# Optimization experiments

Hardware: AMD Instinct MI355X
Metric: run time of the kernel (lower is better)

Reference implementation:

```python
import jax, jax.numpy as jnp
import numpy as np

N, E = 20000, 320000
IN_DIM, EDGE_DIM, HID = 64, 16, 64
# (in_c, heads, channels, out_c) per layer; last layer heads=1, concat=False
DIMS = [(64, 4, 64, 256), (256, 4, 64, 256), (256, 1, 64, 64)]


def _ln(x, g, b):
    m = x.mean(-1, keepdims=True)
    v = x.var(-1, keepdims=True)
    return (x - m) / jnp.sqrt(v + 1e-5) * g + b


def _gatv2(x, ei, ea, Wl, bl, Wr, br, We, att, bc, concat):
    # PyG GATv2Conv, eval mode (no dropout), add_self_loops=True, fill_value='mean'
    n = x.shape[0]
    H, C = att.shape
    ar = jnp.arange(n, dtype=ei.dtype)
    src = jnp.concatenate([ei[0], ar])
    dst = jnp.concatenate([ei[1], ar])
    ea_f = jnp.concatenate([ea, jnp.broadcast_to(ea.mean(0), (n, ea.shape[1]))], 0)
    xl = (x @ Wl + bl).reshape(n, H, C)   # source transform
    xr = (x @ Wr + br).reshape(n, H, C)   # target transform
    ee = (ea_f @ We).reshape(-1, H, C)    # edge transform (no bias in PyG)
    e = jax.nn.leaky_relu(xl[src] + xr[dst] + ee, 0.2)       # [E+N, H, C]
    score = jnp.einsum('ehc,hc->eh', e, att)                 # [E+N, H]
    mx = jax.ops.segment_max(score, dst, num_segments=n)
    a = jnp.exp(score - mx[dst])
    a = a / (jax.ops.segment_sum(a, dst, num_segments=n)[dst] + 1e-16)
    out = jax.ops.segment_sum(a[:, :, None] * xl[src], dst, num_segments=n)  # [N,H,C]
    out = out.reshape(n, H * C) if concat else out.mean(1)
    return out + bc


def _forward(x, eis, eas, Wp, bp, gp, bep, layers):
    h = jax.nn.gelu(_ln(x @ Wp + bp, gp, bep), approximate=False)
    for i in range(3):
        Wl, bl, Wr, br, We, att, bc, g, be, Wsk, bsk = layers[i]
        res = h @ Wsk + bsk
        h = _gatv2(h, eis[i], eas[i], Wl, bl, Wr, br, We, att, bc, i < 2)
        h = jax.nn.gelu(_ln(h, g, be), approximate=False) + res
    return h


def setup_inputs() -> dict:
    key = jax.random.key(0)
    ks = iter(jax.random.split(key, 64))
    rn = lambda shape, s=0.05: jax.random.normal(next(ks), shape, jnp.float32) * s
    d = {'x': jax.random.normal(next(ks), (N, IN_DIM), jnp.float32)}
    for i in range(3):
        d['ei%d' % i] = jax.random.randint(next(ks), (2, E), 0, N, jnp.int32)
        d['ea%d' % i] = jax.random.normal(next(ks), (E, EDGE_DIM), jnp.float32)
    d['Wp'] = rn((IN_DIM, HID)); d['bp'] = jnp.zeros(HID)
    d['gp'] = jnp.ones(HID); d['bep'] = jnp.zeros(HID)
    for i, (ic, H, C, oc) in enumerate(DIMS):
        hc = H * C
        d['Wl%d' % i] = rn((ic, hc)); d['bl%d' % i] = jnp.zeros(hc)
        d['Wr%d' % i] = rn((ic, hc)); d['br%d' % i] = jnp.zeros(hc)
        d['We%d' % i] = rn((EDGE_DIM, hc))
        d['att%d' % i] = rn((H, C), 0.1)
        d['bc%d' % i] = jnp.zeros(hc if i < 2 else C)
        d['g%d' % i] = jnp.ones(oc); d['be%d' % i] = jnp.zeros(oc)
        d['Wsk%d' % i] = rn((ic, oc)); d['bsk%d' % i] = jnp.zeros(oc)
    return d


def reference(x, ei0, ea0, ei1, ea1, ei2, ea2, Wp, bp, gp, bep,
              Wl0, bl0, Wr0, br0, We0, att0, bc0, g0, be0, Wsk0, bsk0,
              Wl1, bl1, Wr1, br1, We1, att1, bc1, g1, be1, Wsk1, bsk1,
              Wl2, bl2, Wr2, br2, We2, att2, bc2, g2, be2, Wsk2, bsk2):
    layers = [
        (Wl0, bl0, Wr0, br0, We0, att0, bc0, g0, be0, Wsk0, bsk0),
        (Wl1, bl1, Wr1, br1, We1, att1, bc1, g1, be1, Wsk1, bsk1),
        (Wl2, bl2, Wr2, br2, We2, att2, bc2, g2, be2, Wsk2, bsk2),
    ]
    return _forward(x, (ei0, ei1, ei2), (ea0, ea1, ea2), Wp, bp, gp, bep, layers)
```

## Files before the change

kernel.cpp:

```cpp
#include <hip/hip_runtime.h>
#include <hip/hip_bf16.h>
#include <math.h>

#define NV 20000
#define NE 320000
#define CSR_PAD 8

typedef __attribute__((ext_vector_type(8))) short bf16x8;
typedef __attribute__((ext_vector_type(4))) float f32x4;
typedef __attribute__((ext_vector_type(2))) _Float16 h2;

static __device__ __forceinline__ ushort f2b(float f) {
  __hip_bfloat16 h = __float2bfloat16(f);
  return *reinterpret_cast<ushort*>(&h);
}
static __device__ __forceinline__ float b2f(ushort u) {
  union { ushort s[2]; float f; } c;
  c.s[0] = 0; c.s[1] = u;
  return c.f;
}
static __device__ __forceinline__ ushort f2h(float f) {
  _Float16 h = (_Float16)f;
  return *reinterpret_cast<ushort*>(&h);
}
static __device__ __forceinline__ float blo(unsigned u) { return __uint_as_float(u << 16); }
static __device__ __forceinline__ float bhi(unsigned u) { return __uint_as_float(u & 0xffff0000u); }

static __device__ __forceinline__ float wave_sum64(float x) {
  x += __int_as_float(__builtin_amdgcn_update_dpp(0, __float_as_int(x), 0x111, 0xF, 0xF, true));
  x += __int_as_float(__builtin_amdgcn_update_dpp(0, __float_as_int(x), 0x112, 0xF, 0xF, true));
  x += __int_as_float(__builtin_amdgcn_update_dpp(0, __float_as_int(x), 0x114, 0xF, 0xF, true));
  x += __int_as_float(__builtin_amdgcn_update_dpp(0, __float_as_int(x), 0x118, 0xF, 0xF, true));
  x += __int_as_float(__builtin_amdgcn_update_dpp(0, __float_as_int(x), 0x142, 0xA, 0xF, true));
  x += __int_as_float(__builtin_amdgcn_update_dpp(0, __float_as_int(x), 0x143, 0xC, 0xF, true));
  return __int_as_float(__builtin_amdgcn_readlane(__float_as_int(x), 63));
}

static __device__ __forceinline__ float sum16(float x) {
  x += __int_as_float(__builtin_amdgcn_update_dpp(0, __float_as_int(x), 0x121, 0xF, 0xF, true));
  x += __int_as_float(__builtin_amdgcn_update_dpp(0, __float_as_int(x), 0x122, 0xF, 0xF, true));
  x += __int_as_float(__builtin_amdgcn_update_dpp(0, __float_as_int(x), 0x124, 0xF, 0xF, true));
  x += __int_as_float(__builtin_amdgcn_update_dpp(0, __float_as_int(x), 0x128, 0xF, 0xF, true));
  return x;
}

static __device__ __forceinline__ float dot16h(const uint4* __restrict__ E,
                                               const h2* __restrict__ Wch) {
#if __has_builtin(__builtin_amdgcn_fdot2)
  const h2* e = (const h2*)E;
  float s = 0.f;
#pragma unroll
  for (int j = 0; j < 8; ++j) s = __builtin_amdgcn_fdot2(e[j], Wch[j], s, false);
  return s;
#else
  const unsigned* u = (const unsigned*)E;
  float s = 0.f;
#pragma unroll
  for (int j = 0; j < 8; ++j) {
    union { unsigned v; h2 h; } cv; cv.v = u[j];
    s = fmaf((float)cv.h[0], (float)Wch[j][0], s);
    s = fmaf((float)cv.h[1], (float)Wch[j][1], s);
  }
  return s;
#endif
}

struct CJob { const float* src; ushort* dst; int K, M; };
struct PrepArgs {
  const int* ei[3];
  const float* ea[3];
  int* counts[3];
  float* easum[3];
  CJob jobs[9];
  const float *x, *Wp, *bp, *gp, *bep;
  ushort* h0;
};

__global__ __launch_bounds__(256) void prep_kernel(PrepArgs a) {
  const int y = blockIdx.y, t = threadIdx.x;
  if (y < 3) {
    if (blockIdx.x < 256) {
      const float4* ea4 = (const float4*)a.ea[y];
      const int cg = t & 3;
      int r = blockIdx.x * 64 + (t >> 2);
      const int rstride = 256 * 64;
      float4 s = make_float4(0.f, 0.f, 0.f, 0.f);
      for (; r < NE; r += rstride) {
        float4 v = ea4[(size_t)r * 4 + cg];
        s.x += v.x; s.y += v.y; s.z += v.z; s.w += v.w;
      }
      __shared__ float4 red4[256];
      red4[t] = s;
      __syncthreads();
      if (t < 4) {
        float4 tot = make_float4(0.f, 0.f, 0.f, 0.f);
        for (int j = t; j < 256; j += 4) {
          float4 v = red4[j];
          tot.x += v.x; tot.y += v.y; tot.z += v.z; tot.w += v.w;
        }
        atomicAdd(&a.easum[y][t * 4 + 0], tot.x);
        atomicAdd(&a.easum[y][t * 4 + 1], tot.y);
        atomicAdd(&a.easum[y][t * 4 + 2], tot.z);
        atomicAdd(&a.easum[y][t * 4 + 3], tot.w);
      }
    }
    int i = blockIdx.x * 256 + t;
    if (i < NE) atomicAdd(&a.counts[y][a.ei[y][NE + i]], 1);
  } else if (y == 3) {
#pragma unroll
    for (int j = 0; j < 9; ++j) {
      CJob jb = a.jobs[j];
      const int total = jb.M * jb.K;
      for (int i = blockIdx.x * 256 + t; i < total; i += gridDim.x * 256) {
        int m = i / jb.K, k = i - m * jb.K;
        jb.dst[i] = f2b(jb.src[(size_t)k * jb.M + m]);
      }
    }
  } else {
    int wid = t >> 6, lane = t & 63;
    for (int row = blockIdx.x * 4 + wid; row < NV; row += gridDim.x * 4) {
      float xv = a.x[(size_t)row * 64 + lane];
      float acc = a.bp[lane];
#pragma unroll
      for (int k = 0; k < 64; ++k) {
        float v = __shfl(xv, k, 64);
        acc = fmaf(v, a.Wp[k * 64 + lane], acc);
      }
      float s1 = wave_sum64(acc), s2 = wave_sum64(acc * acc);
      float mean = s1 * (1.0f / 64.0f);
      float var  = s2 * (1.0f / 64.0f) - mean * mean;
      float yv = (acc - mean) * rsqrtf(var + 1e-5f) * a.gp[lane] + a.bep[lane];
      float gel = 0.5f * yv * (1.0f + erff(yv * 0.70710678118654752f));
      a.h0[(size_t)row * 64 + lane] = f2b(gel);
    }
  }
}

__global__ __launch_bounds__(1024) void scan_kernel(
    int* __restrict__ countsA, int* __restrict__ cursorA)
{
  int* counts = countsA + blockIdx.x * (NV + 1);
  int* cursor = cursorA + blockIdx.x * NV;
  __shared__ int ws[16];
  __shared__ int wexcl[17];
  const int t = threadIdx.x, lane = t & 63, wid = t >> 6;
  const int base = t * 20;
  int v[20];
  int tot = 0;
#pragma unroll
  for (int j = 0; j < 20; ++j) {
    int i = base + j;
    v[j] = (i < NV) ? counts[i] : 0;
    tot += v[j];
  }
  int x = tot;
#pragma unroll
  for (int o = 1; o < 64; o <<= 1) {
    int yy = __shfl_up(x, o, 64);
    if (lane >= o) x += yy;
  }
  if (lane == 63) ws[wid] = x;
  __syncthreads();
  if (t == 0) {
    int r = 0;
#pragma unroll
    for (int j = 0; j < 16; ++j) { wexcl[j] = r; r += ws[j]; }
    wexcl[16] = r;
  }
  __syncthreads();
  int run = wexcl[wid] + (x - tot);
#pragma unroll
  for (int j = 0; j < 20; ++j) {
    int i = base + j;
    if (i < NV) { counts[i] = run; cursor[i] = run; }
    run += v[j];
  }
  if (t == 0) counts[NV] = wexcl[16];
}

struct G0SArgs {
  const ushort *A, *WT;
  const float *b0, *b1, *b2;
  ushort *O0, *O1; float* O2;
  int K, M1, M2, Mtot, NT;
  const int* ei[3]; const float* ea[3];
  int* cursor;
  unsigned* csr[3]; ushort* eab[3]; int HC[3];
};

__global__ __launch_bounds__(256) void gemm0_scatter_kernel(G0SArgs a) {
  __shared__ ushort As[128][40];
  __shared__ ushort Bs[64][40];
  const int t = threadIdx.x;
  if ((int)blockIdx.x < a.NT) {
    const int wave = t >> 6, lane = t & 63;
    const int mcols = a.Mtot >> 6;
    const int col0 = ((int)blockIdx.x % mcols) * 64, row0 = ((int)blockIdx.x / mcols) * 128;
    const int m_ = lane & 15, q = lane >> 4;
    f32x4 acc[2][4];
#pragma unroll
    for (int i = 0; i < 2; ++i)
#pragma unroll
      for (int j = 0; j < 4; ++j) acc[i][j] = (f32x4){0.f, 0.f, 0.f, 0.f};
    const int ar = t >> 1, ac = (t & 1) * 16;
    const int br = t >> 2, bcol = (t & 3) * 8;
    const ushort* Ap = a.A + (size_t)(row0 + ar) * a.K + ac;
    const ushort* Bp = a.WT + (size_t)(col0 + br) * a.K + bcol;
    const bool a_ok = (row0 + ar) < NV;
    for (int k0 = 0; k0 < a.K; k0 += 32) {
      uint4 av0 = make_uint4(0, 0, 0, 0), av1 = make_uint4(0, 0, 0, 0);
      if (a_ok) { av0 = *(const uint4*)(Ap + k0); av1 = *(const uint4*)(Ap + k0 + 8); }
      uint4 bv = *(const uint4*)(Bp + k0);
      *(uint4*)&As[ar][ac] = av0;
      *(uint4*)&As[ar][ac + 8] = av1;
      *(uint4*)&Bs[br][bcol] = bv;
      __syncthreads();
      bf16x8 a0 = *(const bf16x8*)&As[wave * 32 + m_][q * 8];
      bf16x8 a1 = *(const bf16x8*)&As[wave * 32 + 16 + m_][q * 8];
#pragma unroll
      for (int cf = 0; cf < 4; ++cf) {
        bf16x8 b = *(const bf16x8*)&Bs[cf * 16 + m_][q * 8];
        acc[0][cf] = __builtin_amdgcn_mfma_f32_16x16x32_bf16(a0, b, acc[0][cf], 0, 0, 0);
        acc[1][cf] = __builtin_amdgcn_mfma_f32_16x16x32_bf16(a1, b, acc[1][cf], 0, 0, 0);
      }
      __syncthreads();
    }
    const float* bias; int base, mode, Wd;
    if (col0 < a.M1)      { bias = a.b0; base = 0;    mode = 0; Wd = a.M1; }
    else if (col0 < a.M2) { bias = a.b1; base = a.M1; mode = 1; Wd = a.M2 - a.M1; }
    else                  { bias = a.b2; base = a.M2; mode = 2; Wd = a.Mtot - a.M2; }
#pragma unroll
    for (int rf = 0; rf < 2; ++rf) {
#pragma unroll
      for (int cf = 0; cf < 4; ++cf) {
        int col = col0 + cf * 16 + m_ - base;
        float bb = bias[col];
#pragma unroll
        for (int r = 0; r < 4; ++r) {
          int row = row0 + wave * 32 + rf * 16 + q * 4 + r;
          if (row < NV) {
            float v = acc[rf][cf][r] + bb;
            if (mode == 0)      a.O0[(size_t)row * Wd + col] = f2b(v);
            else if (mode == 1) a.O1[(size_t)row * Wd + col] = f2b(v);
            else                a.O2[(size_t)row * Wd + col] = v;
          }
        }
      }
    }
  } else {
    const int per = NE + CSR_PAD;
    int gi = ((int)blockIdx.x - a.NT) * 256 + t;
    if (gi >= 3 * per) return;
    int l = gi / per, i = gi - l * per;
    if (i >= NE) {
      a.csr[l][i] = 0u;
      uint4 z = make_uint4(0, 0, 0, 0);
      *(uint4*)(a.eab[l] + (size_t)i * 16) = z;
      *(uint4*)(a.eab[l] + (size_t)i * 16 + 8) = z;
      return;
    }
    int dst = a.ei[l][NE + i], src = a.ei[l][i];
    int pos = atomicAdd(&a.cursor[(size_t)l * NV + dst], 1);
    a.csr[l][pos] = (unsigned)(src * a.HC[l]);
    const float4* er = (const float4*)(a.ea[l] + (size_t)i * 16);
    float4 q0 = er[0], q1 = er[1], q2 = er[2], q3 = er[3];
    uint4 w0, w1;
    w0.x = (unsigned)f2h(q0.x) | ((unsigned)f2h(q0.y) << 16);
    w0.y = (unsigned)f2h(q0.z) | ((unsigned)f2h(q0.w) << 16);
    w0.z = (unsigned)f2h(q1.x) | ((unsigned)f2h(q1.y) << 16);
    w0.w = (unsigned)f2h(q1.z) | ((unsigned)f2h(q1.w) << 16);
    w1.x = (unsigned)f2h(q2.x) | ((unsigned)f2h(q2.y) << 16);
    w1.y = (unsigned)f2h(q2.z) | ((unsigned)f2h(q2.w) << 16);
    w1.z = (unsigned)f2h(q3.x) | ((unsigned)f2h(q3.y) << 16);
    w1.w = (unsigned)f2h(q3.z) | ((unsigned)f2h(q3.w) << 16);
    *(uint4*)(a.eab[l] + (size_t)pos * 16) = w0;
    *(uint4*)(a.eab[l] + (size_t)pos * 16 + 8) = w1;
  }
}

__global__ __launch_bounds__(256) void gemm_fused(
    const ushort* __restrict__ A, const ushort* __restrict__ WT,
    const float* __restrict__ b0, const float* __restrict__ b1,
    const float* __restrict__ b2,
    ushort* __restrict__ O0, ushort* __restrict__ O1, float* __restrict__ O2,
    int N, int K, int M1, int M2, int Mtot)
{
  __shared__ ushort As[128][40];
  __shared__ ushort Bs[64][40];
  const int t = threadIdx.x, wave = t >> 6, lane = t & 63;
  const int row0 = blockIdx.y * 128, col0 = blockIdx.x * 64;
  const int m_ = lane & 15, q = lane >> 4;
  f32x4 acc[2][4];
#pragma unroll
  for (int i = 0; i < 2; ++i)
#pragma unroll
    for (int j = 0; j < 4; ++j) acc[i][j] = (f32x4){0.f, 0.f, 0.f, 0.f};
  const int ar = t >> 1, ac = (t & 1) * 16;
  const int br = t >> 2, bcol = (t & 3) * 8;
  const ushort* Ap = A + (size_t)(row0 + ar) * K + ac;
  const ushort* Bp = WT + (size_t)(col0 + br) * K + bcol;
  const bool a_ok = (row0 + ar) < N;
  for (int k0 = 0; k0 < K; k0 += 32) {
    uint4 av0 = make_uint4(0, 0, 0, 0), av1 = make_uint4(0, 0, 0, 0);
    if (a_ok) { av0 = *(const uint4*)(Ap + k0); av1 = *(const uint4*)(Ap + k0 + 8); }
    uint4 bv = *(const uint4*)(Bp + k0);
    *(uint4*)&As[ar][ac] = av0;
    *(uint4*)&As[ar][ac + 8] = av1;
    *(uint4*)&Bs[br][bcol] = bv;
    __syncthreads();
    bf16x8 a0 = *(const bf16x8*)&As[wave * 32 + m_][q * 8];
    bf16x8 a1 = *(const bf16x8*)&As[wave * 32 + 16 + m_][q * 8];
#pragma unroll
    for (int cf = 0; cf < 4; ++cf) {
      bf16x8 b = *(const bf16x8*)&Bs[cf * 16 + m_][q * 8];
      acc[0][cf] = __builtin_amdgcn_mfma_f32_16x16x32_bf16(a0, b, acc[0][cf], 0, 0, 0);
      acc[1][cf] = __builtin_amdgcn_mfma_f32_16x16x32_bf16(a1, b, acc[1][cf], 0, 0, 0);
    }
    __syncthreads();
  }
  const float* bias; int base, mode, Wd;
  if (col0 < M1)      { bias = b0; base = 0;  mode = 0; Wd = M1; }
  else if (col0 < M2) { bias = b1; base = M1; mode = 1; Wd = M2 - M1; }
  else                { bias = b2; base = M2; mode = 2; Wd = Mtot - M2; }
#pragma unroll
  for (int rf = 0; rf < 2; ++rf) {
#pragma unroll
    for (int cf = 0; cf < 4; ++cf) {
      int col = col0 + cf * 16 + m_ - base;
      float bb = bias[col];
#pragma unroll
      for (int r = 0; r < 4; ++r) {
        int row = row0 + wave * 32 + rf * 16 + q * 4 + r;
        if (row < N) {
          float v = acc[rf][cf][r] + bb;
          if (mode == 0)      O0[(size_t)row * Wd + col] = f2b(v);
          else if (mode == 1) O1[(size_t)row * Wd + col] = f2b(v);
          else                O2[(size_t)row * Wd + col] = v;
        }
      }
    }
  }
}

__global__ __launch_bounds__(256) void agg4_kernel(
    const ushort* __restrict__ eab, const float* __restrict__ easum,
    const float* __restrict__ We,
    const ushort* __restrict__ xl, const ushort* __restrict__ xr,
    const float* __restrict__ att, const float* __restrict__ bc,
    const float* __restrict__ g, const float* __restrict__ be,
    const float* __restrict__ res,
    const int* __restrict__ offs, const unsigned* __restrict__ csr,
    ushort* __restrict__ houtb, int E)
{
  const int t = threadIdx.x, lane = t & 63, wave = t >> 6;
  const int n = blockIdx.x * 4 + wave;
  const int cb = 4 * lane;
  const size_t rowb = (size_t)n * 256 + cb;
  const float L2E = 1.4426950408889634f;

  float4 atv = *(const float4*)(att + cb);
  float at[4] = {atv.x * L2E, atv.y * L2E, atv.z * L2E, atv.w * L2E};

  h2 Wch[4][8];
  float esf[4] = {0.f, 0.f, 0.f, 0.f};
#pragma unroll
  for (int k = 0; k < 8; ++k) {
    float4 wr0 = *(const float4*)(We + (2 * k) * 256 + cb);
    float4 wr1 = *(const float4*)(We + (2 * k + 1) * 256 + cb);
    const float* w0 = &wr0.x;
    const float* w1 = &wr1.x;
    float e0 = easum[2 * k], e1 = easum[2 * k + 1];
#pragma unroll
    for (int j = 0; j < 4; ++j) {
      esf[j] = fmaf(e0, w0[j], esf[j]);
      esf[j] = fmaf(e1, w1[j], esf[j]);
      Wch[j][k] = (h2){(_Float16)w0[j], (_Float16)w1[j]};
    }
  }
#pragma unroll
  for (int j = 0; j < 4; ++j) esf[j] *= 1.0f / (float)E;

  uint2 qr = *(const uint2*)(xr + rowb);
  float xrv[4] = {blo(qr.x), bhi(qr.x), blo(qr.y), bhi(qr.y)};
  uint2 qn = *(const uint2*)(xl + rowb);
  float xln[4] = {blo(qn.x), bhi(qn.x), blo(qn.y), bhi(qn.y)};

  float p = 0.f;
#pragma unroll
  for (int j = 0; j < 4; ++j) {
    float v = xln[j] + xrv[j] + esf[j];
    v = v > 0.f ? v : 0.2f * v;
    p = fmaf(v, at[j], p);
  }
  float wself = exp2f(sum16(p));
  float acc[4];
#pragma unroll
  for (int j = 0; j < 4; ++j) acc[j] = wself * xln[j];
  float denom = wself;

  const int beg = __builtin_amdgcn_readfirstlane(offs[n]);
  const int end = __builtin_amdgcn_readfirstlane(offs[n + 1]);

  unsigned P[2];
  uint4 EA[2][2];
  uint2 XL[2];
#pragma unroll
  for (int k = 0; k < 2; ++k) {
    P[k] = csr[beg + k];
    const uint4* ep = (const uint4*)(eab + (size_t)(beg + k) * 16);
    EA[k][0] = ep[0]; EA[k][1] = ep[1];
  }
#pragma unroll
  for (int k = 0; k < 2; ++k)
    XL[k] = *(const uint2*)(xl + __builtin_amdgcn_readfirstlane(P[k]) + cb);

  for (int idx = beg; idx < end; idx += 2) {
    unsigned Q[2];
    uint4 EB[2][2];
    uint2 XN[2];
#pragma unroll
    for (int k = 0; k < 2; ++k) Q[k] = csr[idx + 2 + k];
#pragma unroll
    for (int k = 0; k < 2; ++k) {
      const uint4* ep = (const uint4*)(eab + (size_t)(idx + 2 + k) * 16);
      EB[k][0] = ep[0]; EB[k][1] = ep[1];
    }
#pragma unroll
    for (int k = 0; k < 2; ++k)
      XN[k] = *(const uint2*)(xl + __builtin_amdgcn_readfirstlane(Q[k]) + cb);

#pragma unroll
    for (int k = 0; k < 2; ++k) {
      float xf[4] = {blo(XL[k].x), bhi(XL[k].x), blo(XL[k].y), bhi(XL[k].y)};
      float pp = 0.f;
#pragma unroll
      for (int j = 0; j < 4; ++j) {
        float ee = dot16h(EA[k], Wch[j]);
        float v = xf[j] + xrv[j] + ee;
        v = v > 0.f ? v : 0.2f * v;
        pp = fmaf(v, at[j], pp);
      }
      float S = sum16(pp);
      float w = (idx + k < end) ? exp2f(S) : 0.f;
#pragma unroll
      for (int j = 0; j < 4; ++j) acc[j] = fmaf(w, xf[j], acc[j]);
      denom += w;
    }
#pragma unroll
    for (int k = 0; k < 2; ++k) { P[k] = Q[k]; EA[k][0] = EB[k][0]; EA[k][1] = EB[k][1]; XL[k] = XN[k]; }
  }

  const float inv = 1.0f / (denom + 1e-16f);
  float4 bcv = *(const float4*)(bc + cb);
  float out[4];
  out[0] = acc[0] * inv + bcv.x; out[1] = acc[1] * inv + bcv.y;
  out[2] = acc[2] * inv + bcv.z; out[3] = acc[3] * inv + bcv.w;

  float so1 = out[0] + out[1] + out[2] + out[3];
  float so2 = out[0] * out[0] + out[1] * out[1] + out[2] * out[2] + out[3] * out[3];
  float s1 = wave_sum64(so1), s2 = wave_sum64(so2);
  float mean = s1 * (1.0f / 256.0f);
  float var  = s2 * (1.0f / 256.0f) - mean * mean;
  float rstd = rsqrtf(var + 1e-5f);
  float4 gv = *(const float4*)(g + cb);
  float4 bev = *(const float4*)(be + cb);
  float4 rv = *(const float4*)(res + rowb);
  const float* gp = &gv.x; const float* bep = &bev.x; const float* rp = &rv.x;
  ushort ob[4];
#pragma unroll
  for (int j = 0; j < 4; ++j) {
    float y = (out[j] - mean) * rstd * gp[j] + bep[j];
    float gel = 0.5f * y * (1.0f + erff(y * 0.70710678118654752f));
    ob[j] = f2b(gel + rp[j]);
  }
  uint2 ov;
  ov.x = (unsigned)ob[0] | ((unsigned)ob[1] << 16);
  ov.y = (unsigned)ob[2] | ((unsigned)ob[3] << 16);
  *(uint2*)(houtb + rowb) = ov;
}

__global__ __launch_bounds__(256, 4) void agg1_kernel(
    const ushort* __restrict__ eab, const float* __restrict__ easum,
    const float* __restrict__ We,
    const ushort* __restrict__ xl, const ushort* __restrict__ xr,
    const float* __restrict__ att, const float* __restrict__ bc,
    const float* __restrict__ g, const float* __restrict__ be,
    const float* __restrict__ res,
    const int* __restrict__ offs, const unsigned* __restrict__ csr,
    float* __restrict__ houtf, int E)
{
  const int HC = 64;
  const int t = threadIdx.x, lane = t & 63, wave = t >> 6;
  const int n = blockIdx.x * 4 + wave;
  const int c = lane;

  const float xr_t = b2f(xr[(size_t)n * HC + c]);
  const float att_t = att[c] * 1.4426950408889634f;
  float eself = 0.f;
  h2 Wch[8];
#pragma unroll
  for (int j = 0; j < 8; ++j) {
    float w0 = We[(2 * j) * HC + c], w1 = We[(2 * j + 1) * HC + c];
    eself = fmaf(easum[2 * j], w0, eself);
    eself = fmaf(easum[2 * j + 1], w1, eself);
    Wch[j] = (h2){(_Float16)w0, (_Float16)w1};
  }
  eself *= 1.0f / (float)E;

  const float xln = b2f(xl[(size_t)n * HC + c]);
  float vs = xln + xr_t + eself;
  vs = vs > 0.f ? vs : 0.2f * vs;
  const float wself = exp2f(wave_sum64(vs * att_t));
  float acc = wself * xln, denom = wself;

  const int beg = __builtin_amdgcn_readfirstlane(offs[n]);
  const int end = __builtin_amdgcn_readfirstlane(offs[n + 1]);

  unsigned P[4];
  uint4 EA[4][2];
  float XL[4];
#pragma unroll
  for (int k = 0; k < 4; ++k) {
    P[k] = csr[beg + k];
    const uint4* ep = (const uint4*)(eab + (size_t)(beg + k) * 16);
    EA[k][0] = ep[0]; EA[k][1] = ep[1];
  }
#pragma unroll
  for (int k = 0; k < 4; ++k)
    XL[k] = b2f(xl[__builtin_amdgcn_readfirstlane(P[k]) + c]);

  for (int idx = beg; idx < end; idx += 4) {
    unsigned Q[4];
    uint4 EB[4][2];
    float XLN[4];
#pragma unroll
    for (int k = 0; k < 4; ++k) Q[k] = csr[idx + 4 + k];
#pragma unroll
    for (int k = 0; k < 4; ++k) {
      const uint4* ep = (const uint4*)(eab + (size_t)(idx + 4 + k) * 16);
      EB[k][0] = ep[0]; EB[k][1] = ep[1];
    }
#pragma unroll
    for (int k = 0; k < 4; ++k)
      XLN[k] = b2f(xl[__builtin_amdgcn_readfirstlane(Q[k]) + c]);

    float wv[4];
#pragma unroll
    for (int k = 0; k < 4; ++k) {
      float ee = dot16h(EA[k], Wch);
      float v = XL[k] + xr_t + ee;
      v = v > 0.f ? v : 0.2f * v;
      float S = wave_sum64(v * att_t);
      wv[k] = (idx + k < end) ? exp2f(S) : 0.f;
    }
#pragma unroll
    for (int k = 0; k < 4; ++k) { acc = fmaf(wv[k], XL[k], acc); denom += wv[k]; }
#pragma unroll
    for (int k = 0; k < 4; ++k) {
      P[k] = Q[k]; EA[k][0] = EB[k][0]; EA[k][1] = EB[k][1]; XL[k] = XLN[k];
    }
  }

  float out = acc / (denom + 1e-16f) + bc[c];
  float s1 = wave_sum64(out), s2 = wave_sum64(out * out);
  float mean = s1 / (float)HC;
  float var  = s2 / (float)HC - mean * mean;
  float y = (out - mean) * rsqrtf(var + 1e-5f) * g[c] + be[c];
  float gel = 0.5f * y * (1.0f + erff(y * 0.70710678118654752f));
  houtf[(size_t)n * HC + c] = gel + res[(size_t)n * HC + c];
}

extern "C" void kernel_launch(void* const* d_in, const int* in_sizes, int n_in,
                              void* d_out, int out_size, void* d_ws, size_t ws_size,
                              hipStream_t stream)
{
  auto in = [&](int i) { return (const float*)d_in[i]; };

  const int ic[3] = {64, 256, 256}, hc[3] = {256, 256, 64}, oc[3] = {256, 256, 64};
  const int CSRN = NE + CSR_PAD;

  char* w = (char*)d_ws;
  size_t off = 0;
  auto alloc = [&](size_t bytes) { void* p = w + off; off = (off + bytes + 511) & ~(size_t)511; return p; };
  ushort* B1   = (ushort*)alloc((size_t)NV * 256 * 2);
  ushort* B2   = (ushort*)alloc((size_t)NV * 256 * 2);
  float*  B3   = (float*)alloc((size_t)NV * 256 * 4);
  ushort* h0bf = (ushort*)alloc((size_t)NV * 64 * 2);
  ushort* h1bf = (ushort*)alloc((size_t)NV * 256 * 2);
  ushort* h2bf = (ushort*)alloc((size_t)NV * 256 * 2);
  ushort* Wcat[3];
  for (int i = 0; i < 3; ++i)
    Wcat[i] = (ushort*)alloc((size_t)(2 * hc[i] + oc[i]) * ic[i] * 2);
  float*    easumA  = (float*)alloc(3 * 64);
  int*      countsA = (int*)alloc((size_t)3 * (NV + 1) * 4);
  int*      cursorA = (int*)alloc((size_t)3 * NV * 4);
  unsigned* csrA    = (unsigned*)alloc((size_t)3 * CSRN * 4);
  ushort*   eabA    = (ushort*)alloc((size_t)3 * CSRN * 16 * 2);

  hipMemsetAsync(easumA, 0, 512 + (size_t)3 * (NV + 1) * 4, stream);

  PrepArgs pa;
  for (int i = 0; i < 3; ++i) {
    pa.ei[i] = (const int*)d_in[1 + 2 * i];
    pa.ea[i] = in(2 + 2 * i);
    pa.counts[i] = countsA + i * (NV + 1);
    pa.easum[i] = easumA + i * 16;
    pa.jobs[i * 3 + 0] = {in(11 + 11 * i), Wcat[i],                             ic[i], hc[i]};
    pa.jobs[i * 3 + 1] = {in(13 + 11 * i), Wcat[i] + (size_t)hc[i] * ic[i],     ic[i], hc[i]};
    pa.jobs[i * 3 + 2] = {in(20 + 11 * i), Wcat[i] + (size_t)2 * hc[i] * ic[i], ic[i], oc[i]};
  }
  pa.x = in(0); pa.Wp = in(7); pa.bp = in(8); pa.gp = in(9); pa.bep = in(10);
  pa.h0 = h0bf;
  prep_kernel<<<dim3(1344, 5), 256, 0, stream>>>(pa);

  scan_kernel<<<3, 1024, 0, stream>>>(countsA, cursorA);

  G0SArgs ga;
  ga.A = h0bf; ga.WT = Wcat[0];
  ga.b0 = in(12); ga.b1 = in(14); ga.b2 = in(21);
  ga.O0 = B1; ga.O1 = B2; ga.O2 = B3;
  ga.K = 64; ga.M1 = 256; ga.M2 = 512; ga.Mtot = 768;
  ga.NT = (768 / 64) * ((NV + 127) / 128);
  for (int i = 0; i < 3; ++i) {
    ga.ei[i] = (const int*)d_in[1 + 2 * i];
    ga.ea[i] = in(2 + 2 * i);
    ga.csr[i] = csrA + (size_t)i * CSRN;
    ga.eab[i] = eabA + (size_t)i * CSRN * 16;
    ga.HC[i] = hc[i];
  }
  ga.cursor = cursorA;
  const int scat_blocks = (3 * (NE + CSR_PAD) + 255) / 256;
  gemm0_scatter_kernel<<<ga.NT + scat_blocks, 256, 0, stream>>>(ga);

  agg4_kernel<<<NV / 4, 256, 0, stream>>>(
      eabA + 0, easumA + 0, in(15), B1, B2, in(16), in(17), in(18), in(19),
      B3, countsA, csrA, h1bf, NE);

  gemm_fused<<<dim3(768 / 64, (NV + 127) / 128), 256, 0, stream>>>(
      h1bf, Wcat[1], in(23), in(25), in(32), B1, B2, B3, NV, 256, 256, 512, 768);

  agg4_kernel<<<NV / 4, 256, 0, stream>>>(
      eabA + (size_t)CSRN * 16, easumA + 16, in(26), B1, B2, in(27), in(28),
      in(29), in(30), B3, countsA + (NV + 1), csrA + (size_t)CSRN, h2bf, NE);

  gemm_fused<<<dim3(192 / 64, (NV + 127) / 128), 256, 0, stream>>>(
      h2bf, Wcat[2], in(34), in(36), in(43), B1, B2, B3, NV, 256, 64, 128, 192);

  agg1_kernel<<<NV / 4, 256, 0, stream>>>(
      eabA + (size_t)2 * CSRN * 16, easumA + 32, in(37), B1, B2, in(38), in(39),
      in(40), in(41), B3, countsA + 2 * (NV + 1), csrA + (size_t)2 * CSRN,
      (float*)d_out, NE);
}
```

Measured before the change: 539.4 us.

## Keep edge features in original order and gather them via CSR-stored edge ids

```diff
diff --git a/kernel.cpp b/kernel.cpp
--- a/kernel.cpp
+++ b/kernel.cpp
@@ -4,7 +4,7 @@
 
 #define NV 20000
 #define NE 320000
-#define CSR_PAD 8
+#define CSR_PAD 16
 
 typedef __attribute__((ext_vector_type(8))) short bf16x8;
 typedef __attribute__((ext_vector_type(4))) float f32x4;
@@ -71,6 +71,7 @@
   const float* ea[3];
   int* counts[3];
   float* easum[3];
+  ushort* eab[3];
   CJob jobs[9];
   const float *x, *Wp, *bp, *gp, *bep;
   ushort* h0;
@@ -81,6 +82,7 @@
   if (y < 3) {
     if (blockIdx.x < 256) {
       const float4* ea4 = (const float4*)a.ea[y];
+      ushort* eab = a.eab[y];
       const int cg = t & 3;
       int r = blockIdx.x * 64 + (t >> 2);
       const int rstride = 256 * 64;
@@ -88,6 +90,10 @@
       for (; r < NE; r += rstride) {
         float4 v = ea4[(size_t)r * 4 + cg];
         s.x += v.x; s.y += v.y; s.z += v.z; s.w += v.w;
+        uint2 w;
+        w.x = (unsigned)f2h(v.x) | ((unsigned)f2h(v.y) << 16);
+        w.y = (unsigned)f2h(v.z) | ((unsigned)f2h(v.w) << 16);
+        *(uint2*)(eab + (size_t)r * 16 + cg * 4) = w;
       }
       __shared__ float4 red4[256];
       red4[t] = s;
@@ -183,9 +189,9 @@
   const float *b0, *b1, *b2;
   ushort *O0, *O1; float* O2;
   int K, M1, M2, Mtot, NT;
-  const int* ei[3]; const float* ea[3];
+  const int* ei[3];
   int* cursor;
-  unsigned* csr[3]; ushort* eab[3]; int HC[3];
+  uint2* csr[3]; int HC[3];
 };
 
 __global__ __launch_bounds__(256) void gemm0_scatter_kernel(G0SArgs a) {
@@ -253,28 +259,12 @@
     if (gi >= 3 * per) return;
     int l = gi / per, i = gi - l * per;
     if (i >= NE) {
-      a.csr[l][i] = 0u;
-      uint4 z = make_uint4(0, 0, 0, 0);
-      *(uint4*)(a.eab[l] + (size_t)i * 16) = z;
-      *(uint4*)(a.eab[l] + (size_t)i * 16 + 8) = z;
+      a.csr[l][i] = make_uint2(0u, 0u);
       return;
     }
     int dst = a.ei[l][NE + i], src = a.ei[l][i];
     int pos = atomicAdd(&a.cursor[(size_t)l * NV + dst], 1);
-    a.csr[l][pos] = (unsigned)(src * a.HC[l]);
-    const float4* er = (const float4*)(a.ea[l] + (size_t)i * 16);
-    float4 q0 = er[0], q1 = er[1], q2 = er[2], q3 = er[3];
-    uint4 w0, w1;
-    w0.x = (unsigned)f2h(q0.x) | ((unsigned)f2h(q0.y) << 16);
-    w0.y = (unsigned)f2h(q0.z) | ((unsigned)f2h(q0.w) << 16);
-    w0.z = (unsigned)f2h(q1.x) | ((unsigned)f2h(q1.y) << 16);
-    w0.w = (unsigned)f2h(q1.z) | ((unsigned)f2h(q1.w) << 16);
-    w1.x = (unsigned)f2h(q2.x) | ((unsigned)f2h(q2.y) << 16);
-    w1.y = (unsigned)f2h(q2.z) | ((unsigned)f2h(q2.w) << 16);
-    w1.z = (unsigned)f2h(q3.x) | ((unsigned)f2h(q3.y) << 16);
-    w1.w = (unsigned)f2h(q3.z) | ((unsigned)f2h(q3.w) << 16);
-    *(uint4*)(a.eab[l] + (size_t)pos * 16) = w0;
-    *(uint4*)(a.eab[l] + (size_t)pos * 16 + 8) = w1;
+    a.csr[l][pos] = make_uint2((unsigned)(src * a.HC[l]), (unsigned)i);
   }
 }
 
@@ -349,7 +339,7 @@
     const float* __restrict__ att, const float* __restrict__ bc,
     const float* __restrict__ g, const float* __restrict__ be,
     const float* __restrict__ res,
-    const int* __restrict__ offs, const unsigned* __restrict__ csr,
+    const int* __restrict__ offs, const uint2* __restrict__ csr,
     ushort* __restrict__ houtb, int E)
 {
   const int t = threadIdx.x, lane = t & 63, wave = t >> 6;
@@ -401,33 +391,37 @@
   const int beg = __builtin_amdgcn_readfirstlane(offs[n]);
   const int end = __builtin_amdgcn_readfirstlane(offs[n + 1]);
 
-  unsigned P[2];
+  uint2 QS[2];
   uint4 EA[2][2];
   uint2 XL[2];
-#pragma unroll
-  for (int k = 0; k < 2; ++k) {
-    P[k] = csr[beg + k];
-    const uint4* ep = (const uint4*)(eab + (size_t)(beg + k) * 16);
-    EA[k][0] = ep[0]; EA[k][1] = ep[1];
-  }
-#pragma unroll
-  for (int k = 0; k < 2; ++k)
-    XL[k] = *(const uint2*)(xl + __builtin_amdgcn_readfirstlane(P[k]) + cb);
+  {
+    uint2 Q0[2];
+#pragma unroll
+    for (int k = 0; k < 2; ++k) Q0[k] = csr[beg + k];
+#pragma unroll
+    for (int k = 0; k < 2; ++k) QS[k] = csr[beg + 2 + k];
+#pragma unroll
+    for (int k = 0; k < 2; ++k) {
+      const uint4* ep = (const uint4*)(eab +
+          (size_t)__builtin_amdgcn_readfirstlane(Q0[k].y) * 16);
+      EA[k][0] = ep[0]; EA[k][1] = ep[1];
+      XL[k] = *(const uint2*)(xl + __builtin_amdgcn_readfirstlane(Q0[k].x) + cb);
+    }
+  }
 
   for (int idx = beg; idx < end; idx += 2) {
-    unsigned Q[2];
+    uint2 QN[2];
+#pragma unroll
+    for (int k = 0; k < 2; ++k) QN[k] = csr[idx + 4 + k];
     uint4 EB[2][2];
     uint2 XN[2];
 #pragma unroll
-    for (int k = 0; k < 2; ++k) Q[k] = csr[idx + 2 + k];
-#pragma unroll
     for (int k = 0; k < 2; ++k) {
-      const uint4* ep = (const uint4*)(eab + (size_t)(idx + 2 + k) * 16);
+      const uint4* ep = (const uint4*)(eab +
+          (size_t)__builtin_amdgcn_readfirstlane(QS[k].y) * 16);
       EB[k][0] = ep[0]; EB[k][1] = ep[1];
-    }
-#pragma unroll
-    for (int k = 0; k < 2; ++k)
-      XN[k] = *(const uint2*)(xl + __builtin_amdgcn_readfirstlane(Q[k]) + cb);
+      XN[k] = *(const uint2*)(xl + __builtin_amdgcn_readfirstlane(QS[k].x) + cb);
+    }
 
 #pragma unroll
     for (int k = 0; k < 2; ++k) {
@@ -447,7 +441,9 @@
       denom += w;
     }
 #pragma unroll
-    for (int k = 0; k < 2; ++k) { P[k] = Q[k]; EA[k][0] = EB[k][0]; EA[k][1] = EB[k][1]; XL[k] = XN[k]; }
+    for (int k = 0; k < 2; ++k) {
+      EA[k][0] = EB[k][0]; EA[k][1] = EB[k][1]; XL[k] = XN[k]; QS[k] = QN[k];
+    }
   }
 
   const float inv = 1.0f / (denom + 1e-16f);
@@ -486,7 +482,7 @@
     const float* __restrict__ att, const float* __restrict__ bc,
     const float* __restrict__ g, const float* __restrict__ be,
     const float* __restrict__ res,
-    const int* __restrict__ offs, const unsigned* __restrict__ csr,
+    const int* __restrict__ offs, const uint2* __restrict__ csr,
     float* __restrict__ houtf, int E)
 {
   const int HC = 64;
@@ -516,33 +512,41 @@
   const int beg = __builtin_amdgcn_readfirstlane(offs[n]);
   const int end = __builtin_amdgcn_readfirstlane(offs[n + 1]);
 
-  unsigned P[4];
+  uint2 QS[4];
   uint4 EA[4][2];
   float XL[4];
-#pragma unroll
-  for (int k = 0; k < 4; ++k) {
-    P[k] = csr[beg + k];
-    const uint4* ep = (const uint4*)(eab + (size_t)(beg + k) * 16);
-    EA[k][0] = ep[0]; EA[k][1] = ep[1];
-  }
-#pragma unroll
-  for (int k = 0; k < 4; ++k)
-    XL[k] = b2f(xl[__builtin_amdgcn_readfirstlane(P[k]) + c]);
+  {
+    uint2 Q0[4];
+#pragma unroll
+    for (int k = 0; k < 4; ++k) Q0[k] = csr[beg + k];
+#pragma unroll
+    for (int k = 0; k < 4; ++k) QS[k] = csr[beg + 4 + k];
+#pragma unroll
+    for (int k = 0; k < 4; ++k) {
+      const uint4* ep = (const uint4*)(eab +
+          (size_t)__builtin_amdgcn_readfirstlane(Q0[k].y) * 16);
+      EA[k][0] = ep[0]; EA[k][1] = ep[1];
+    }
+#pragma unroll
+    for (int k = 0; k < 4; ++k)
+      XL[k] = b2f(xl[__builtin_amdgcn_readfirstlane(Q0[k].x) + c]);
+  }
 
   for (int idx = beg; idx < end; idx += 4) {
-    unsigned Q[4];
+    uint2 QN[4];
+#pragma unroll
+    for (int k = 0; k < 4; ++k) QN[k] = csr[idx + 8 + k];
     uint4 EB[4][2];
     float XLN[4];
 #pragma unroll
-    for (int k = 0; k < 4; ++k) Q[k] = csr[idx + 4 + k];
-#pragma unroll
     for (int k = 0; k < 4; ++k) {
-      const uint4* ep = (const uint4*)(eab + (size_t)(idx + 4 + k) * 16);
+      const uint4* ep = (const uint4*)(eab +
+          (size_t)__builtin_amdgcn_readfirstlane(QS[k].y) * 16);
       EB[k][0] = ep[0]; EB[k][1] = ep[1];
     }
 #pragma unroll
     for (int k = 0; k < 4; ++k)
-      XLN[k] = b2f(xl[__builtin_amdgcn_readfirstlane(Q[k]) + c]);
+      XLN[k] = b2f(xl[__builtin_amdgcn_readfirstlane(QS[k].x) + c]);
 
     float wv[4];
 #pragma unroll
@@ -557,7 +561,7 @@
     for (int k = 0; k < 4; ++k) { acc = fmaf(wv[k], XL[k], acc); denom += wv[k]; }
 #pragma unroll
     for (int k = 0; k < 4; ++k) {
-      P[k] = Q[k]; EA[k][0] = EB[k][0]; EA[k][1] = EB[k][1]; XL[k] = XLN[k];
+      EA[k][0] = EB[k][0]; EA[k][1] = EB[k][1]; XL[k] = XLN[k]; QS[k] = QN[k];
     }
   }
 
@@ -594,8 +598,8 @@
   float*    easumA  = (float*)alloc(3 * 64);
   int*      countsA = (int*)alloc((size_t)3 * (NV + 1) * 4);
   int*      cursorA = (int*)alloc((size_t)3 * NV * 4);
-  unsigned* csrA    = (unsigned*)alloc((size_t)3 * CSRN * 4);
-  ushort*   eabA    = (ushort*)alloc((size_t)3 * CSRN * 16 * 2);
+  uint2*    csr2A   = (uint2*)alloc((size_t)3 * CSRN * sizeof(uint2));
+  ushort*   eab16A  = (ushort*)alloc((size_t)3 * NE * 16 * 2);
 
   hipMemsetAsync(easumA, 0, 512 + (size_t)3 * (NV + 1) * 4, stream);
 
@@ -605,6 +609,7 @@
     pa.ea[i] = in(2 + 2 * i);
     pa.counts[i] = countsA + i * (NV + 1);
     pa.easum[i] = easumA + i * 16;
+    pa.eab[i] = eab16A + (size_t)i * NE * 16;
     pa.jobs[i * 3 + 0] = {in(11 + 11 * i), Wcat[i],                             ic[i], hc[i]};
     pa.jobs[i * 3 + 1] = {in(13 + 11 * i), Wcat[i] + (size_t)hc[i] * ic[i],     ic[i], hc[i]};
     pa.jobs[i * 3 + 2] = {in(20 + 11 * i), Wcat[i] + (size_t)2 * hc[i] * ic[i], ic[i], oc[i]};
@@ -623,9 +628,7 @@
   ga.NT = (768 / 64) * ((NV + 127) / 128);
   for (int i = 0; i < 3; ++i) {
     ga.ei[i] = (const int*)d_in[1 + 2 * i];
-    ga.ea[i] = in(2 + 2 * i);
-    ga.csr[i] = csrA + (size_t)i * CSRN;
-    ga.eab[i] = eabA + (size_t)i * CSRN * 16;
+    ga.csr[i] = csr2A + (size_t)i * CSRN;
     ga.HC[i] = hc[i];
   }
   ga.cursor = cursorA;
@@ -633,21 +636,21 @@
   gemm0_scatter_kernel<<<ga.NT + scat_blocks, 256, 0, stream>>>(ga);
 
   agg4_kernel<<<NV / 4, 256, 0, stream>>>(
-      eabA + 0, easumA + 0, in(15), B1, B2, in(16), in(17), in(18), in(19),
-      B3, countsA, csrA, h1bf, NE);
+      eab16A, easumA + 0, in(15), B1, B2, in(16), in(17), in(18), in(19),
+      B3, countsA, csr2A, h1bf, NE);
 
   gemm_fused<<<dim3(768 / 64, (NV + 127) / 128), 256, 0, stream>>>(
       h1bf, Wcat[1], in(23), in(25), in(32), B1, B2, B3, NV, 256, 256, 512, 768);
 
   agg4_kernel<<<NV / 4, 256, 0, stream>>>(
-      eabA + (size_t)CSRN * 16, easumA + 16, in(26), B1, B2, in(27), in(28),
-      in(29), in(30), B3, countsA + (NV + 1), csrA + (size_t)CSRN, h2bf, NE);
+      eab16A + (size_t)NE * 16, easumA + 16, in(26), B1, B2, in(27), in(28),
+      in(29), in(30), B3, countsA + (NV + 1), csr2A + (size_t)CSRN, h2bf, NE);
 
   gemm_fused<<<dim3(192 / 64, (NV + 127) / 128), 256, 0, stream>>>(
       h2bf, Wcat[2], in(34), in(36), in(43), B1, B2, B3, NV, 256, 64, 128, 192);
 
   agg1_kernel<<<NV / 4, 256, 0, stream>>>(
-      eabA + (size_t)2 * CSRN * 16, easumA + 32, in(37), B1, B2, in(38), in(39),
-      in(40), in(41), B3, countsA + 2 * (NV + 1), csrA + (size_t)2 * CSRN,
+      eab16A + (size_t)2 * NE * 16, easumA + 32, in(37), B1, B2, in(38), in(39),
+      in(40), in(41), B3, countsA + 2 * (NV + 1), csr2A + (size_t)2 * CSRN,
       (float*)d_out, NE);
 }
```

After: 564.5 us. +4.7%, slower.

## Record per-edge rank during counting to replace scatter-phase cursor atomics

Applied to the files above, without the earlier changes.

```diff
diff --git a/kernel.cpp b/kernel.cpp
--- a/kernel.cpp
+++ b/kernel.cpp
@@ -4,7 +4,7 @@
 
 #define NV 20000
 #define NE 320000
-#define CSR_PAD 8
+#define CSR_PAD 16
 
 typedef __attribute__((ext_vector_type(8))) short bf16x8;
 typedef __attribute__((ext_vector_type(4))) float f32x4;
@@ -71,6 +71,7 @@
   const float* ea[3];
   int* counts[3];
   float* easum[3];
+  ushort* rank[3];
   CJob jobs[9];
   const float *x, *Wp, *bp, *gp, *bep;
   ushort* h0;
@@ -79,11 +80,11 @@
 __global__ __launch_bounds__(256) void prep_kernel(PrepArgs a) {
   const int y = blockIdx.y, t = threadIdx.x;
   if (y < 3) {
-    if (blockIdx.x < 256) {
+    if (blockIdx.x < 512) {
       const float4* ea4 = (const float4*)a.ea[y];
       const int cg = t & 3;
       int r = blockIdx.x * 64 + (t >> 2);
-      const int rstride = 256 * 64;
+      const int rstride = 512 * 64;
       float4 s = make_float4(0.f, 0.f, 0.f, 0.f);
       for (; r < NE; r += rstride) {
         float4 v = ea4[(size_t)r * 4 + cg];
@@ -104,8 +105,17 @@
         atomicAdd(&a.easum[y][t * 4 + 3], tot.w);
       }
     }
-    int i = blockIdx.x * 256 + t;
-    if (i < NE) atomicAdd(&a.counts[y][a.ei[y][NE + i]], 1);
+    int e = blockIdx.x * 256 + t;
+    if (e < NE / 4) {
+      int4 d4 = *(const int4*)(a.ei[y] + NE + e * 4);
+      int* cnt = a.counts[y];
+      ushort4 rk;
+      rk.x = (ushort)atomicAdd(&cnt[d4.x], 1);
+      rk.y = (ushort)atomicAdd(&cnt[d4.y], 1);
+      rk.z = (ushort)atomicAdd(&cnt[d4.z], 1);
+      rk.w = (ushort)atomicAdd(&cnt[d4.w], 1);
+      *(ushort4*)(a.rank[y] + e * 4) = rk;
+    }
   } else if (y == 3) {
 #pragma unroll
     for (int j = 0; j < 9; ++j) {
@@ -137,10 +147,10 @@
 }
 
 __global__ __launch_bounds__(1024) void scan_kernel(
-    int* __restrict__ countsA, int* __restrict__ cursorA)
+    const int* __restrict__ countsA, int* __restrict__ offsA)
 {
-  int* counts = countsA + blockIdx.x * (NV + 1);
-  int* cursor = cursorA + blockIdx.x * NV;
+  const int* counts = countsA + blockIdx.x * (NV + 1);
+  int* offs = offsA + blockIdx.x * (NV + 1);
   __shared__ int ws[16];
   __shared__ int wexcl[17];
   const int t = threadIdx.x, lane = t & 63, wid = t >> 6;
@@ -172,10 +182,10 @@
 #pragma unroll
   for (int j = 0; j < 20; ++j) {
     int i = base + j;
-    if (i < NV) { counts[i] = run; cursor[i] = run; }
+    if (i < NV) offs[i] = run;
     run += v[j];
   }
-  if (t == 0) counts[NV] = wexcl[16];
+  if (t == 0) offs[NV] = wexcl[16];
 }
 
 struct G0SArgs {
@@ -184,7 +194,8 @@
   ushort *O0, *O1; float* O2;
   int K, M1, M2, Mtot, NT;
   const int* ei[3]; const float* ea[3];
-  int* cursor;
+  const int* offs;
+  const ushort* rank;
   unsigned* csr[3]; ushort* eab[3]; int HC[3];
 };
 
@@ -260,7 +271,7 @@
       return;
     }
     int dst = a.ei[l][NE + i], src = a.ei[l][i];
-    int pos = atomicAdd(&a.cursor[(size_t)l * NV + dst], 1);
+    int pos = a.offs[l * (NV + 1) + dst] + (int)a.rank[(size_t)l * NE + i];
     a.csr[l][pos] = (unsigned)(src * a.HC[l]);
     const float4* er = (const float4*)(a.ea[l] + (size_t)i * 16);
     float4 q0 = er[0], q1 = er[1], q2 = er[2], q3 = er[3];
@@ -593,7 +604,8 @@
     Wcat[i] = (ushort*)alloc((size_t)(2 * hc[i] + oc[i]) * ic[i] * 2);
   float*    easumA  = (float*)alloc(3 * 64);
   int*      countsA = (int*)alloc((size_t)3 * (NV + 1) * 4);
-  int*      cursorA = (int*)alloc((size_t)3 * NV * 4);
+  int*      offsA   = (int*)alloc((size_t)3 * (NV + 1) * 4);
+  ushort*   rankA   = (ushort*)alloc((size_t)3 * NE * 2);
   unsigned* csrA    = (unsigned*)alloc((size_t)3 * CSRN * 4);
   ushort*   eabA    = (ushort*)alloc((size_t)3 * CSRN * 16 * 2);
 
@@ -605,6 +617,7 @@
     pa.ea[i] = in(2 + 2 * i);
     pa.counts[i] = countsA + i * (NV + 1);
     pa.easum[i] = easumA + i * 16;
+    pa.rank[i] = rankA + (size_t)i * NE;
     pa.jobs[i * 3 + 0] = {in(11 + 11 * i), Wcat[i],                             ic[i], hc[i]};
     pa.jobs[i * 3 + 1] = {in(13 + 11 * i), Wcat[i] + (size_t)hc[i] * ic[i],     ic[i], hc[i]};
     pa.jobs[i * 3 + 2] = {in(20 + 11 * i), Wcat[i] + (size_t)2 * hc[i] * ic[i], ic[i], oc[i]};
@@ -613,7 +626,7 @@
   pa.h0 = h0bf;
   prep_kernel<<<dim3(1344, 5), 256, 0, stream>>>(pa);
 
-  scan_kernel<<<3, 1024, 0, stream>>>(countsA, cursorA);
+  scan_kernel<<<3, 1024, 0, stream>>>(countsA, offsA);
 
   G0SArgs ga;
   ga.A = h0bf; ga.WT = Wcat[0];
@@ -628,26 +641,27 @@
     ga.eab[i] = eabA + (size_t)i * CSRN * 16;
     ga.HC[i] = hc[i];
   }
-  ga.cursor = cursorA;
+  ga.offs = offsA;
+  ga.rank = rankA;
   const int scat_blocks = (3 * (NE + CSR_PAD) + 255) / 256;
   gemm0_scatter_kernel<<<ga.NT + scat_blocks, 256, 0, stream>>>(ga);
 
   agg4_kernel<<<NV / 4, 256, 0, stream>>>(
       eabA + 0, easumA + 0, in(15), B1, B2, in(16), in(17), in(18), in(19),
-      B3, countsA, csrA, h1bf, NE);
+      B3, offsA, csrA, h1bf, NE);
 
   gemm_fused<<<dim3(768 / 64, (NV + 127) / 128), 256, 0, stream>>>(
       h1bf, Wcat[1], in(23), in(25), in(32), B1, B2, B3, NV, 256, 256, 512, 768);
 
   agg4_kernel<<<NV / 4, 256, 0, stream>>>(
       eabA + (size_t)CSRN * 16, easumA + 16, in(26), B1, B2, in(27), in(28),
-      in(29), in(30), B3, countsA + (NV + 1), csrA + (size_t)CSRN, h2bf, NE);
+      in(29), in(30), B3, offsA + (NV + 1), csrA + (size_t)CSRN, h2bf, NE);
 
   gemm_fused<<<dim3(192 / 64, (NV + 127) / 128), 256, 0, stream>>>(
       h2bf, Wcat[2], in(34), in(36), in(43), B1, B2, B3, NV, 256, 64, 128, 192);
 
   agg1_kernel<<<NV / 4, 256, 0, stream>>>(
       eabA + (size_t)2 * CSRN * 16, easumA + 32, in(37), B1, B2, in(38), in(39),
-      in(40), in(41), B3, countsA + 2 * (NV + 1), csrA + (size_t)2 * CSRN,
+      in(40), in(41), B3, offsA + 2 * (NV + 1), csrA + (size_t)2 * CSRN,
       (float*)d_out, NE);
 }
```

Measured after the change: 540.3 us. About the same (+0.2%).
